# Kernel tuning notes

Hardware: AMD Instinct MI355X
Metric: run time of the kernel (lower is better)

## Reference

```python
import jax, jax.numpy as jnp
import numpy as np

B, L, T = 32, 512, 400
EMB, PRE, ENC, ARNN, DRNN, NSYM = 512, 256, 512, 1024, 1024, 256
MEAN_COEFF, SCALE_COEFF = 1.0, 10.0


def setup_inputs() -> dict:
    key = jax.random.key(0)
    ks = jax.random.split(key, 20)
    s = 0.02
    inp = {
        'memory': jax.random.normal(ks[0], (B, L, ENC), jnp.float32),
        'decoder_inputs': jax.random.normal(ks[1], (B, EMB, T), jnp.float32),
        'memory_lengths': jax.random.randint(ks[2], (B,), L // 2, L + 1).astype(jnp.int64),
        # prenet
        'pW1': jax.random.normal(ks[3], (PRE, EMB), jnp.float32) * s,
        'pb1': jnp.zeros((PRE,), jnp.float32),
        'pW2': jax.random.normal(ks[4], (PRE, PRE), jnp.float32) * s,
        'pb2': jnp.zeros((PRE,), jnp.float32),
        # attention LSTMCell
        'aWih': jax.random.normal(ks[5], (4 * ARNN, PRE + ENC), jnp.float32) * s,
        'aWhh': jax.random.normal(ks[6], (4 * ARNN, ARNN), jnp.float32) * s,
        'abih': jnp.zeros((4 * ARNN,), jnp.float32),
        'abhh': jnp.zeros((4 * ARNN,), jnp.float32),
        # Gaussian attention param linear (weight zero-init in torch; small here)
        'attWp': jax.random.normal(ks[7], (2, ARNN), jnp.float32) * 0.001,
        'attbp': jnp.zeros((2,), jnp.float32),
        # decoder LSTMCell
        'dWih': jax.random.normal(ks[8], (4 * DRNN, ARNN + ENC), jnp.float32) * s,
        'dWhh': jax.random.normal(ks[9], (4 * DRNN, DRNN), jnp.float32) * s,
        'dbih': jnp.zeros((4 * DRNN,), jnp.float32),
        'dbhh': jnp.zeros((4 * DRNN,), jnp.float32),
        # output linear
        'oW': jax.random.normal(ks[10], (NSYM, DRNN + ENC), jnp.float32) * s,
        'ob': jnp.zeros((NSYM,), jnp.float32),
    }
    return inp


def _lstm_cell(x, h, c, Wih, Whh, bih, bhh):
    g = x @ Wih.T + bih + h @ Whh.T + bhh
    i, f, gg, o = jnp.split(g, 4, axis=-1)
    c = jax.nn.sigmoid(f) * c + jax.nn.sigmoid(i) * jnp.tanh(gg)
    h = jax.nn.sigmoid(o) * jnp.tanh(c)
    return h, c


def _decoder_core(memory, decoder_inputs, memory_lengths,
                  pW1, pb1, pW2, pb2,
                  aWih, aWhh, abih, abhh,
                  attWp, attbp,
                  dWih, dWhh, dbih, dbhh,
                  oW, ob):
    b = memory.shape[0]
    Lm = memory.shape[1]
    # go frame + time-major inputs -> prenet (dropout is identity in eval)
    x = jnp.transpose(decoder_inputs, (2, 0, 1))            # [T, B, EMB]
    x = jnp.concatenate([jnp.zeros((1, b, EMB), x.dtype), x], axis=0)  # [T+1, B, EMB]
    x = jax.nn.relu(x @ pW1.T + pb1)
    x = jax.nn.relu(x @ pW2.T + pb2)                        # [T+1, B, PRE]
    x = x[:T]                                               # loop runs T steps

    lin = jnp.arange(Lm, dtype=memory.dtype)[None, :]       # [1, L]
    pad_mask = lin >= memory_lengths[:, None].astype(memory.dtype)  # [B, L] True at pad

    def step(carry, x_t):
        ah, ac, dh, dc, ctx, mean = carry
        cell_in = jnp.concatenate([x_t, ctx], axis=1)
        ah, ac = _lstm_cell(cell_in, ah, ac, aWih, aWhh, abih, abhh)
        params = ah @ attWp.T + attbp                       # [B, 2]
        mean = mean + jnp.exp(params[:, 0:1]) * MEAN_COEFF  # [B, 1]
        scale = jnp.exp(params[:, 1:2]) * SCALE_COEFF       # [B, 1]
        Z = jnp.sqrt(2.0 * np.pi * scale ** 2)
        w = jnp.exp(-0.5 * (lin - mean) ** 2 / scale ** 2) / Z  # [B, L]
        w = jnp.where(pad_mask, 0.0, w)
        ctx = jnp.einsum('bl,bld->bd', w, memory)           # [B, ENC]
        dec_in = jnp.concatenate([ah, ctx], axis=1)
        dh, dc = _lstm_cell(dec_in, dh, dc, dWih, dWhh, dbih, dbhh)
        out = jnp.concatenate([dh, ctx], axis=1) @ oW.T + ob  # [B, NSYM]
        return (ah, ac, dh, dc, ctx, mean), (out, w, params)

    z = jnp.zeros
    carry0 = (z((b, ARNN)), z((b, ARNN)), z((b, DRNN)), z((b, DRNN)),
              z((b, ENC)), z((b, 1)))
    _, (logits, aligns, ps) = jax.lax.scan(step, carry0, x)
    # time-major -> [B, T, ...]
    return (jnp.transpose(logits, (1, 0, 2)),
            jnp.transpose(aligns, (1, 0, 2)),
            jnp.transpose(ps, (1, 0, 2)))


def reference(memory, decoder_inputs, memory_lengths,
              pW1, pb1, pW2, pb2,
              aWih, aWhh, abih, abhh,
              attWp, attbp,
              dWih, dWhh, dbih, dbhh,
              oW, ob):
    return _decoder_core(memory, decoder_inputs, memory_lengths,
                         pW1, pb1, pW2, pb2,
                         aWih, aWhh, abih, abhh,
                         attWp, attbp,
                         dWih, dWhh, dbih, dbhh,
                         oW, ob)
```

## Files before the change

kernel.cpp:

```cpp
#include <hip/hip_runtime.h>
#include <math.h>

#define Bsz   32
#define Lmem  512
#define Tsteps 400
#define EMBD  512
#define PRE   256
#define ENCD  512
#define ARNN  1024
#define DRNN  1024
#define NSYM  256

typedef _Float16 f16x8 __attribute__((ext_vector_type(8)));
typedef float    f32x4 __attribute__((ext_vector_type(4)));
typedef _Float16 half_t;

#define KA2  (PRE + ENCD + ARNN)
#define KA2Q (KA2 / 4)
#define NMA2 (KA2Q / 32)
#define KD2  (ARNN + ENCD + DRNN)
#define KD2Q (KD2 / 4)
#define NMD2 (KD2Q / 32)
#define LDA_A2 1800
#define LDA_D2 2568

#define KA1  1280
#define KA1Q 320
#define NMA1 10
#define KD1  2048
#define KD1Q 512
#define NMD1 16
#define LDA_A1 1288
#define LDA_D1 2056
#define WCAP 216

__device__ __forceinline__ void st_agent_f16(half_t* p, half_t v) {
    __hip_atomic_store((unsigned short*)p, __builtin_bit_cast(unsigned short, v),
                       __ATOMIC_RELAXED, __HIP_MEMORY_SCOPE_AGENT);
}
__device__ __forceinline__ void st_agent_f32(float* p, float v) {
    __hip_atomic_store(p, v, __ATOMIC_RELAXED, __HIP_MEMORY_SCOPE_AGENT);
}
__device__ __forceinline__ void st_agent_u32(unsigned* p, unsigned v) {
    __hip_atomic_store(p, v, __ATOMIC_RELAXED, __HIP_MEMORY_SCOPE_AGENT);
}
__device__ __forceinline__ void st_agent_u64(unsigned long long* p, unsigned long long v) {
    __hip_atomic_store(p, v, __ATOMIC_RELAXED, __HIP_MEMORY_SCOPE_AGENT);
}
__device__ __forceinline__ float ld_agent_f32(const float* p) {
    return __hip_atomic_load(p, __ATOMIC_RELAXED, __HIP_MEMORY_SCOPE_AGENT);
}
__device__ __forceinline__ unsigned ld_agent_u32(const unsigned* p) {
    return __hip_atomic_load(p, __ATOMIC_RELAXED, __HIP_MEMORY_SCOPE_AGENT);
}
__device__ __forceinline__ unsigned long long ld_agent_u64(const unsigned long long* p) {
    return __hip_atomic_load(p, __ATOMIC_RELAXED, __HIP_MEMORY_SCOPE_AGENT);
}
__device__ __forceinline__ f16x8 ld_agent_f16x8(const half_t* p) {
    union { unsigned long long u[2]; f16x8 v; } c;
    c.u[0] = __hip_atomic_load((const unsigned long long*)p,
                               __ATOMIC_RELAXED, __HIP_MEMORY_SCOPE_AGENT);
    c.u[1] = __hip_atomic_load(((const unsigned long long*)p) + 1,
                               __ATOMIC_RELAXED, __HIP_MEMORY_SCOPE_AGENT);
    return c.v;
}
__device__ __forceinline__ void keep16(f16x8& v) { asm volatile("" : "+v"(v)); }

template<int KIH, int KHH>
__global__ __launch_bounds__(256) void conv_lstm_cat(
    const float* __restrict__ Wih, const float* __restrict__ Whh,
    const float* __restrict__ bih, const float* __restrict__ bhh,
    half_t* __restrict__ Wcat, float* __restrict__ bsum)
{
    constexpr int K = KIH + KHH;
    const int j = blockIdx.x;
    const float* srcA = Wih + (size_t)j * KIH;
    const float* srcB = Whh + (size_t)j * KHH;
    half_t* dst = Wcat + (size_t)j * K;
    for (int k = threadIdx.x; k < KIH; k += 256) dst[k]       = (half_t)srcA[k];
    for (int k = threadIdx.x; k < KHH; k += 256) dst[KIH + k] = (half_t)srcB[k];
    if (threadIdx.x == 0) bsum[j] = bih[j] + bhh[j];
}
template<int KIH, int KHH, int L0>
__global__ __launch_bounds__(256) void conv_lstm_skip(
    const float* __restrict__ Wih, const float* __restrict__ Whh,
    const float* __restrict__ bih, const float* __restrict__ bhh,
    half_t* __restrict__ Wcat, float* __restrict__ bsum)
{
    constexpr int K = L0 + KHH;
    const int j = blockIdx.x;
    const float* srcA = Wih + (size_t)j * KIH;
    const float* srcB = Whh + (size_t)j * KHH;
    half_t* dst = Wcat + (size_t)j * K;
    for (int k = threadIdx.x; k < L0; k += 256)  dst[k] = (half_t)srcA[k];
    for (int k = threadIdx.x; k < KHH; k += 256) dst[L0 + k] = (half_t)srcB[k];
    if (threadIdx.x == 0) bsum[j] = bih[j] + bhh[j];
}
__global__ __launch_bounds__(256) void conv_slice(
    const float* __restrict__ src, half_t* __restrict__ dst,
    int srcstride, int off, int cols)
{
    const int r = blockIdx.x;
    for (int k = threadIdx.x; k < cols; k += 256)
        dst[(size_t)r * cols + k] = (half_t)src[(size_t)r * srcstride + off + k];
}
__global__ __launch_bounds__(256) void conv_mat(
    const float* __restrict__ src, half_t* __restrict__ dst, int n)
{
    for (int i = blockIdx.x * 256 + threadIdx.x; i < n; i += gridDim.x * 256)
        dst[i] = (half_t)src[i];
}

__global__ __launch_bounds__(256) void pproj_kernel(
    const float* __restrict__ Wsrc, int Wstride, int Woff,
    const float* __restrict__ mem, half_t* __restrict__ P)
{
    const int bidx = blockIdx.x;
    const int jt  = bidx >> 9;
    const int rem = bidx & 511;
    const int lt  = rem >> 5;
    const int b   = rem & 31;
    const int tid = threadIdx.x;
    const int wave = tid >> 6, lane = tid & 63;
    const int wj = wave >> 1, wl = wave & 1;
    const int m15 = lane & 15, kh = lane >> 4;
    const int j0 = jt * 32 + wj * 16;
    const int l0 = lt * 32 + wl * 16;

    const float* wrow = Wsrc + (size_t)(j0 + m15) * Wstride + Woff + (kh << 3);
    const float* mrow = mem + ((size_t)b * Lmem + (l0 + m15)) * ENCD + (kh << 3);
    f32x4 acc = {0.f, 0.f, 0.f, 0.f};
    for (int k = 0; k < 512; k += 32) {
        float4 w0 = *(const float4*)(wrow + k);
        float4 w1 = *(const float4*)(wrow + k + 4);
        f16x8 av;
        av[0] = (half_t)w0.x; av[1] = (half_t)w0.y; av[2] = (half_t)w0.z; av[3] = (half_t)w0.w;
        av[4] = (half_t)w1.x; av[5] = (half_t)w1.y; av[6] = (half_t)w1.z; av[7] = (half_t)w1.w;
        float4 m0 = *(const float4*)(mrow + k);
        float4 m1 = *(const float4*)(mrow + k + 4);
        f16x8 bv;
        bv[0] = (half_t)m0.x; bv[1] = (half_t)m0.y; bv[2] = (half_t)m0.z; bv[3] = (half_t)m0.w;
        bv[4] = (half_t)m1.x; bv[5] = (half_t)m1.y; bv[6] = (half_t)m1.z; bv[7] = (half_t)m1.w;
        acc = __builtin_amdgcn_mfma_f32_16x16x32_f16(av, bv, acc, 0, 0, 0);
    }
    const int col = lane & 15;
    #pragma unroll
    for (int r = 0; r < 4; ++r) {
        const int row = (kh << 2) + r;
        P[((size_t)(j0 + row) * 32 + b) * 512 + (l0 + col)] = (half_t)acc[r];
    }
}

__global__ __launch_bounds__(256) void prenet_kernel(
    const float* __restrict__ din,
    const float* __restrict__ pW1, const float* __restrict__ pb1,
    const float* __restrict__ pW2, const float* __restrict__ pb2,
    half_t* __restrict__ xpre)
{
    __shared__ float xs[8][EMBD];
    __shared__ float h1s[8][PRE];
    const int tid = threadIdx.x;
    const int row0 = blockIdx.x * 8;

    for (int idx = tid; idx < 8 * EMBD; idx += 256) {
        int r = idx >> 9;
        int e = idx & 511;
        int rid = row0 + r;
        int t = rid >> 5;
        int b = rid & 31;
        float v = 0.f;
        if (t > 0) v = din[(size_t)b * EMBD * Tsteps + (size_t)e * Tsteps + (t - 1)];
        xs[r][e] = v;
    }
    __syncthreads();
    {
        float acc[8] = {0.f,0.f,0.f,0.f,0.f,0.f,0.f,0.f};
        const float* wr = pW1 + (size_t)tid * EMBD;
        for (int e = 0; e < EMBD; e += 4) {
            float4 wv = *(const float4*)(wr + e);
            #pragma unroll
            for (int r = 0; r < 8; ++r) {
                float4 xv = *(const float4*)&xs[r][e];
                acc[r] += wv.x * xv.x + wv.y * xv.y + wv.z * xv.z + wv.w * xv.w;
            }
        }
        float bias = pb1[tid];
        #pragma unroll
        for (int r = 0; r < 8; ++r) h1s[r][tid] = fmaxf(acc[r] + bias, 0.f);
    }
    __syncthreads();
    {
        float acc[8] = {0.f,0.f,0.f,0.f,0.f,0.f,0.f,0.f};
        const float* wr = pW2 + (size_t)tid * PRE;
        for (int e = 0; e < PRE; e += 4) {
            float4 wv = *(const float4*)(wr + e);
            #pragma unroll
            for (int r = 0; r < 8; ++r) {
                float4 xv = *(const float4*)&h1s[r][e];
                acc[r] += wv.x * xv.x + wv.y * xv.y + wv.z * xv.z + wv.w * xv.w;
            }
        }
        float bias = pb2[tid];
        #pragma unroll
        for (int r = 0; r < 8; ++r) {
            int rid = row0 + r;
            int t = rid >> 5;
            int b = rid & 31;
            xpre[(size_t)t * Bsz * PRE + (size_t)b * PRE + tid] =
                (half_t)fmaxf(acc[r] + bias, 0.f);
        }
    }
}

__device__ __forceinline__ void g_arrive(unsigned* flags, unsigned ph)
{
    asm volatile("s_waitcnt vmcnt(0)" ::: "memory");
    __syncthreads();
    if (threadIdx.x == 0)
        st_agent_u32(flags + blockIdx.x * 16, ph);
}
__device__ __forceinline__ void g_wait(unsigned* flags, unsigned ph)
{
    if (threadIdx.x < 64) {
        const unsigned* f = flags + threadIdx.x * 64;
        for (;;) {
            unsigned a = ld_agent_u32(f);
            unsigned b = ld_agent_u32(f + 16);
            unsigned c = ld_agent_u32(f + 32);
            unsigned d = ld_agent_u32(f + 48);
            if (min(min(a, b), min(c, d)) >= ph) break;
            __builtin_amdgcn_s_sleep(2);
        }
    }
    __syncthreads();
}

__global__ __launch_bounds__(512, 1) void decoder_2bar(
    const half_t* __restrict__ Wcat_a, const float* __restrict__ bsum_a,
    const half_t* __restrict__ Wcat_d, const float* __restrict__ bsum_d,
    const half_t* __restrict__ Wo, const float* __restrict__ ob,
    const half_t* __restrict__ xpre,
    const float* __restrict__ attWp, const float* __restrict__ attbp,
    const int* __restrict__ mlen, const half_t* __restrict__ mem16,
    half_t* __restrict__ ah0, half_t* __restrict__ ah1,
    half_t* __restrict__ dh0, half_t* __restrict__ dh1,
    half_t* __restrict__ ctx0, half_t* __restrict__ ctx1,
    float* __restrict__ mean0, float* __restrict__ mean1,
    float* __restrict__ logits, float* __restrict__ aligns,
    float* __restrict__ ps,
    unsigned* flags)
{
    const int blk   = blockIdx.x;
    const int tid   = threadIdx.x;
    const int wave  = tid >> 6;
    const int lane  = tid & 63;
    const int btile = wave & 1;
    const int kq    = wave >> 1;
    const int m15   = lane & 15;
    const int kh    = lane >> 4;
    const int u0    = blk << 2;
    const int bb    = (btile << 4) + m15;

    __shared__ __align__(16) half_t wAl[16 * LDA_A2];
    __shared__ __align__(16) half_t wDl[16 * LDA_D2];
    __shared__ float gredA[4][2][16][16];
    __shared__ float gredD[4][2][16][16];
    __shared__ float wsh[Lmem];
    __shared__ float lred[16][33];
    __shared__ float wred8[8][2];
    __shared__ float bc2[2];

    for (int g = tid; g < 16 * (KA2 / 8); g += 512) {
        int r = g / (KA2 / 8);
        int c = (g - r * (KA2 / 8)) * 8;
        int jr = (r >> 2) * 1024 + u0 + (r & 3);
        *(f16x8*)(wAl + r * LDA_A2 + c) = *(const f16x8*)(Wcat_a + (size_t)jr * KA2 + c);
    }
    for (int g = tid; g < 16 * (KD2 / 8); g += 512) {
        int r = g / (KD2 / 8);
        int c = (g - r * (KD2 / 8)) * 8;
        int jr = (r >> 2) * 1024 + u0 + (r & 3);
        *(f16x8*)(wDl + r * LDA_D2 + c) = *(const f16x8*)(Wcat_d + (size_t)jr * KD2 + c);
    }
    float bsA[4] = {0.f,0.f,0.f,0.f}, bsD[4] = {0.f,0.f,0.f,0.f};
    float cA = 0.f, cD = 0.f;
    if (tid < 128) {
        const int ul = tid >> 5;
        #pragma unroll
        for (int gi = 0; gi < 4; ++gi) bsA[gi] = bsum_a[gi * 1024 + u0 + ul];
    } else if (tid < 256) {
        const int ul = (tid - 128) >> 5;
        #pragma unroll
        for (int gi = 0; gi < 4; ++gi) bsD[gi] = bsum_d[gi * 1024 + u0 + ul];
    }
    const half_t* lA = wAl + m15 * LDA_A2 + kq * KA2Q + (kh << 3);
    const half_t* lD = wDl + m15 * LDA_D2 + kq * KD2Q + (kh << 3);
    __syncthreads();

    f16x8 bvA[NMA2], bvD[NMD2];
    {
        const half_t* s0 = xpre;
        #pragma unroll
        for (int i = 0; i < NMA2; ++i) {
            const int kg = kq * KA2Q + i * 32 + (kh << 3);
            if (kg < PRE)             bvA[i] = *(const f16x8*)(s0 + bb * PRE + kg);
            else if (kg < PRE + ENCD) bvA[i] = ld_agent_f16x8(ctx1 + bb * ENCD + (kg - PRE));
            else                      bvA[i] = ld_agent_f16x8(ah1 + bb * ARNN + (kg - PRE - ENCD));
        }
    }

    unsigned ph = 0;

    for (int t = 0; t <= Tsteps; ++t) {
        const int par = t & 1;
        half_t*       ah_cur  = par ? ah1 : ah0;
        half_t*       ctx_cur = par ? ctx1 : ctx0;
        const half_t* ctx_prv = par ? ctx0 : ctx1;
        float*        mn_cur  = par ? mean1 : mean0;
        const float*  mn_prv  = par ? mean0 : mean1;
        half_t*       dh_s    = par ? dh0 : dh1;

        if (t < Tsteps) {
            f32x4 accA = {0.f,0.f,0.f,0.f};
            #pragma unroll
            for (int i = 0; i < NMA2; ++i) {
                f16x8 av = *(const f16x8*)(lA + i * 32);
                accA = __builtin_amdgcn_mfma_f32_16x16x32_f16(av, bvA[i], accA, 0, 0, 0);
            }
            #pragma unroll
            for (int r = 0; r < 4; ++r)
                gredA[kq][btile][(kh << 2) + r][m15] = accA[r];
        }
        if (t > 0) {
            f32x4 accD = {0.f,0.f,0.f,0.f};
            #pragma unroll
            for (int i = 0; i < NMD2; ++i) {
                f16x8 av = *(const f16x8*)(lD + i * 32);
                accD = __builtin_amdgcn_mfma_f32_16x16x32_f16(av, bvD[i], accD, 0, 0, 0);
            }
            #pragma unroll
            for (int r = 0; r < 4; ++r)
                gredD[kq][btile][(kh << 2) + r][m15] = accD[r];
        }
        __syncthreads();
        if (tid < 128) {
            if (t < Tsteps) {
                const int ul = tid >> 5;
                const int bq = tid & 31;
                const int bt = bq >> 4;
                const int nn = bq & 15;
                float g[4];
                #pragma unroll
                for (int gi = 0; gi < 4; ++gi) {
                    const int mr = (gi << 2) + ul;
                    g[gi] = gredA[0][bt][mr][nn] + gredA[1][bt][mr][nn]
                          + gredA[2][bt][mr][nn] + gredA[3][bt][mr][nn] + bsA[gi];
                }
                float si = 1.f / (1.f + expf(-g[0]));
                float sf = 1.f / (1.f + expf(-g[1]));
                float so = 1.f / (1.f + expf(-g[3]));
                cA = sf * cA + si * tanhf(g[2]);
                st_agent_f16(&ah_cur[bq * 1024 + u0 + ul], (half_t)(so * tanhf(cA)));
            }
        } else if (tid < 256) {
            if (t > 0) {
                const int lt = tid - 128;
                const int ul = lt >> 5;
                const int bq = lt & 31;
                const int bt = bq >> 4;
                const int nn = bq & 15;
                float g[4];
                #pragma unroll
                for (int gi = 0; gi < 4; ++gi) {
                    const int mr = (gi << 2) + ul;
                    g[gi] = gredD[0][bt][mr][nn] + gredD[1][bt][mr][nn]
                          + gredD[2][bt][mr][nn] + gredD[3][bt][mr][nn] + bsD[gi];
                }
                float si = 1.f / (1.f + expf(-g[0]));
                float sf = 1.f / (1.f + expf(-g[1]));
                float so = 1.f / (1.f + expf(-g[3]));
                cD = sf * cD + si * tanhf(g[2]);
                st_agent_f16(&dh_s[bq * 1024 + u0 + ul], (half_t)(so * tanhf(cD)));
            }
        }
        ++ph; g_arrive(flags, ph); g_wait(flags, ph);

        if (t < Tsteps) {
            const int abt = blk >> 3;
            const int dt  = blk & 7;
            float p0, p1;
            {
                union { unsigned u; _Float16 h[2]; } a;
                a.u = ld_agent_u32((const unsigned*)(ah_cur + abt * ARNN + 2 * tid));
                float a0 = (float)a.h[0], a1 = (float)a.h[1];
                float2 w0 = *(const float2*)(attWp + 2 * tid);
                float2 w1 = *(const float2*)(attWp + ARNN + 2 * tid);
                p0 = a0 * w0.x + a1 * w0.y;
                p1 = a0 * w1.x + a1 * w1.y;
            }
            #pragma unroll
            for (int off = 32; off > 0; off >>= 1) {
                p0 += __shfl_down(p0, off, 64);
                p1 += __shfl_down(p1, off, 64);
            }
            if (lane == 0) { wred8[wave][0] = p0; wred8[wave][1] = p1; }
            __syncthreads();
            if (tid == 0) {
                float q0 = attbp[0], q1 = attbp[1];
                #pragma unroll
                for (int w = 0; w < 8; ++w) { q0 += wred8[w][0]; q1 += wred8[w][1]; }
                float mn = ld_agent_f32(&mn_prv[abt]) + expf(q0) * 1.0f;
                float sc = expf(q1) * 10.0f;
                if (dt == 0) {
                    st_agent_f32(&mn_cur[abt], mn);
                    st_agent_f32(&ps[(size_t)abt * Tsteps * 2 + (size_t)t * 2 + 0], q0);
                    st_agent_f32(&ps[(size_t)abt * Tsteps * 2 + (size_t)t * 2 + 1], q1);
                }
                bc2[0] = mn; bc2[1] = sc;
            }
            __syncthreads();
            const float mn = bc2[0], sc = bc2[1];
            const float inv_s = 1.f / sc;
            const float coef = 0.3989422804014327f * inv_s;
            const int len = mlen[abt];
            {
                float z = ((float)tid - mn) * inv_s;
                float wv = (tid < len) ? expf(-0.5f * z * z) * coef : 0.f;
                wsh[tid] = wv;
                if (dt == 0)
                    st_agent_f32(&aligns[(size_t)abt * Tsteps * Lmem + (size_t)t * Lmem + tid], wv);
            }
            __syncthreads();
            int lo = (int)fmaxf(0.f, floorf(mn - 9.f * sc));
            int hi = (int)fminf((float)len, ceilf(mn + 9.f * sc) + 1.f);
            const int d8 = (dt << 6) + (wave << 3);
            const half_t* mb = mem16 + (size_t)abt * Lmem * ENCD + d8;
            float acc[8] = {0.f,0.f,0.f,0.f,0.f,0.f,0.f,0.f};
            for (int l = lo + lane; l < hi; l += 64) {
                f16x8 mv = *(const f16x8*)(mb + (size_t)l * ENCD);
                float w = wsh[l];
                #pragma unroll
                for (int j = 0; j < 8; ++j) acc[j] += w * (float)mv[j];
            }
            #pragma unroll
            for (int off = 32; off > 0; off >>= 1) {
                #pragma unroll
                for (int j = 0; j < 8; ++j) acc[j] += __shfl_down(acc[j], off, 64);
            }
            if (lane == 0) {
                #pragma unroll
                for (int j = 0; j < 4; ++j) {
                    union { unsigned u; _Float16 h[2]; } pk;
                    pk.h[0] = (_Float16)acc[2 * j];
                    pk.h[1] = (_Float16)acc[2 * j + 1];
                    __hip_atomic_store((unsigned*)(ctx_cur + abt * ENCD + d8 + 2 * j), pk.u,
                                       __ATOMIC_RELAXED, __HIP_MEMORY_SCOPE_AGENT);
                }
            }
        }
        if (t > 0) {
            const int b_o = tid & 31;
            const int ks  = tid >> 5;
            const half_t* wrow = Wo + (size_t)blk * (DRNN + ENCD) + ks * 96;
            float outacc = 0.f;
            #pragma unroll
            for (int half = 0; half < 2; ++half) {
                f16x8 wv[6], av[6];
                #pragma unroll
                for (int c8 = 0; c8 < 6; ++c8) {
                    const int cc = half * 6 + c8;
                    const int k = ks * 96 + cc * 8;
                    wv[c8] = *(const f16x8*)(wrow + cc * 8);
                    const half_t* ap = (k < DRNN) ? (dh_s + b_o * DRNN + k)
                                                  : (ctx_prv + b_o * ENCD + (k - DRNN));
                    av[c8] = ld_agent_f16x8(ap);
                }
                #pragma unroll
                for (int c8 = 0; c8 < 6; ++c8)
                    #pragma unroll
                    for (int e = 0; e < 8; ++e)
                        outacc += (float)wv[c8][e] * (float)av[c8][e];
            }
            lred[ks][b_o] = outacc;
            __syncthreads();
            if (tid < 32) {
                float s = 0.f;
                #pragma unroll
                for (int q = 0; q < 16; ++q) s += lred[q][tid];
                st_agent_f32(&logits[(size_t)tid * Tsteps * NSYM + (size_t)(t - 1) * NSYM + blk],
                             s + ob[blk]);
            }
        }
        if (t < Tsteps) {
            ++ph; g_arrive(flags, ph);
            if (t + 1 < Tsteps) {
                const half_t* s0n = xpre + (size_t)(t + 1) * Bsz * PRE;
                #pragma unroll
                for (int i = 0; i < NMA2; ++i) {
                    const int kg = kq * KA2Q + i * 32 + (kh << 3);
                    if (kg < PRE)
                        bvA[i] = *(const f16x8*)(s0n + bb * PRE + kg);
                    else if (kg >= PRE + ENCD)
                        bvA[i] = ld_agent_f16x8(ah_cur + bb * ARNN + (kg - PRE - ENCD));
                }
            }
            #pragma unroll
            for (int i = 0; i < NMD2; ++i) {
                const int kg = kq * KD2Q + i * 32 + (kh << 3);
                if (kg < ARNN)
                    bvD[i] = ld_agent_f16x8(ah_cur + bb * ARNN + kg);
                else if (kg >= ARNN + ENCD)
                    bvD[i] = ld_agent_f16x8(dh_s + bb * DRNN + (kg - ARNN - ENCD));
            }
            #pragma unroll
            for (int i = 0; i < NMA2; ++i) keep16(bvA[i]);
            #pragma unroll
            for (int i = 0; i < NMD2; ++i) keep16(bvD[i]);
            g_wait(flags, ph);
            if (t + 1 < Tsteps) {
                #pragma unroll
                for (int i = 0; i < NMA2; ++i) {
                    const int kg = kq * KA2Q + i * 32 + (kh << 3);
                    if (kg >= PRE && kg < PRE + ENCD)
                        bvA[i] = ld_agent_f16x8(ctx_cur + bb * ENCD + (kg - PRE));
                }
            }
            #pragma unroll
            for (int i = 0; i < NMD2; ++i) {
                const int kg = kq * KD2Q + i * 32 + (kh << 3);
                if (kg >= ARNN && kg < ARNN + ENCD)
                    bvD[i] = ld_agent_f16x8(ctx_cur + bb * ENCD + (kg - ARNN));
            }
        }
    }
}

__global__ __launch_bounds__(512, 2) void decoder_1bar(
    const half_t* __restrict__ Wcat_a, const float* __restrict__ bsum_a,
    const half_t* __restrict__ Wcat_d, const float* __restrict__ bsum_d,
    const half_t* __restrict__ Wo, const float* __restrict__ ob,
    const half_t* __restrict__ xpre,
    const float* __restrict__ attWp, const float* __restrict__ attbp,
    const int* __restrict__ mlen,
    const half_t* __restrict__ P_a, const half_t* __restrict__ P_d,
    const half_t* __restrict__ P_o,
    half_t* __restrict__ ah,
    half_t* __restrict__ dh0, half_t* __restrict__ dh1,
    float* __restrict__ partials,
    float* __restrict__ logits, float* __restrict__ aligns,
    float* __restrict__ ps,
    unsigned* flags)
{
    const int blk   = blockIdx.x;
    const int tid   = threadIdx.x;
    const int wave  = tid >> 6;
    const int lane  = tid & 63;
    const int btile = wave & 1;
    const int kq    = wave >> 1;
    const int m15   = lane & 15;
    const int kh    = lane >> 4;
    const int u0    = blk << 2;
    const int bb    = (btile << 4) + m15;

    __shared__ __align__(16) half_t wAl[16 * LDA_A1];
    __shared__ __align__(16) half_t wDl[16 * LDA_D1];
    __shared__ float gredA[4][2][16][16];
    __shared__ float gredD[4][2][16][16];
    __shared__ float wshc[32][WCAP + 8];
    __shared__ float ctxA[16][32];
    __shared__ float ctxD[16][32];
    __shared__ float ctxO[32];
    __shared__ float lred[16][33];
    __shared__ float part[4][32][2];
    __shared__ float praw[32][2];
    __shared__ float bcc[32][4];
    __shared__ float bcp[32][4];
    __shared__ int   lacur[32], hicur[32];
    __shared__ int   lapv[32], hipv[32];
    __shared__ float mean32[32];
    __shared__ half_t hstA[4][32], hstD[4][32];

    for (int g = tid; g < 16 * (KA1 / 8); g += 512) {
        int r = g / (KA1 / 8);
        int c = (g - r * (KA1 / 8)) * 8;
        int jr = (r >> 2) * 1024 + u0 + (r & 3);
        *(f16x8*)(wAl + r * LDA_A1 + c) = *(const f16x8*)(Wcat_a + (size_t)jr * KA1 + c);
    }
    for (int g = tid; g < 16 * (KD1 / 8); g += 512) {
        int r = g / (KD1 / 8);
        int c = (g - r * (KD1 / 8)) * 8;
        int jr = (r >> 2) * 1024 + u0 + (r & 3);
        *(f16x8*)(wDl + r * LDA_D1 + c) = *(const f16x8*)(Wcat_d + (size_t)jr * KD1 + c);
    }
    float bsA[4] = {0.f,0.f,0.f,0.f}, bsD[4] = {0.f,0.f,0.f,0.f};
    float wp0 = 0.f, wp1 = 0.f;
    float cA = 0.f, cD = 0.f;
    if (tid < 128) {
        const int ul = tid >> 5;
        #pragma unroll
        for (int gi = 0; gi < 4; ++gi) bsA[gi] = bsum_a[gi * 1024 + u0 + ul];
        wp0 = attWp[u0 + ul];
        wp1 = attWp[ARNN + u0 + ul];
    } else if (tid < 256) {
        const int ul = (tid - 128) >> 5;
        #pragma unroll
        for (int gi = 0; gi < 4; ++gi) bsD[gi] = bsum_d[gi * 1024 + u0 + ul];
    }
    if (tid < 32) mean32[tid] = 0.f;
    const half_t* lA = wAl + m15 * LDA_A1 + kq * KA1Q + (kh << 3);
    const half_t* lD = wDl + m15 * LDA_D1 + kq * KD1Q + (kh << 3);
    __syncthreads();

    f16x8 bvA[NMA1], bvD[NMD1];
    #pragma unroll
    for (int i = 0; i < NMA1; ++i) {
        const int kg = kq * KA1Q + i * 32 + (kh << 3);
        if (kg < PRE) bvA[i] = *(const f16x8*)(xpre + bb * PRE + kg);
        else          bvA[i] = ld_agent_f16x8(ah + bb * ARNN + (kg - PRE));
    }

    unsigned ph = 0;

    for (int tau = 0; tau <= Tsteps + 1; ++tau) {
        const int par = tau & 1;
        half_t*       dhW = par ? dh1 : dh0;
        const half_t* dhR = par ? dh0 : dh1;

        if (tau >= 1) {
            if (tid < 32) {
                bcp[tid][0] = bcc[tid][0]; bcp[tid][1] = bcc[tid][1]; bcp[tid][2] = bcc[tid][2];
                lapv[tid] = lacur[tid]; hipv[tid] = hicur[tid];
            }
            __syncthreads();
        }
        if (tau >= 1 && tau <= Tsteps) {
            {
                const int b = tid >> 4, c = tid & 15;
                const unsigned long long* pb =
                    (const unsigned long long*)(partials + ((size_t)b * 256 + c * 16) * 2);
                float s0 = 0.f, s1 = 0.f;
                #pragma unroll
                for (int q = 0; q < 16; ++q) {
                    union { unsigned long long u; float2 f; } v;
                    v.u = ld_agent_u64(pb + q);
                    s0 += v.f.x; s1 += v.f.y;
                }
                s0 += __shfl_down(s0, 8, 16); s1 += __shfl_down(s1, 8, 16);
                s0 += __shfl_down(s0, 4, 16); s1 += __shfl_down(s1, 4, 16);
                s0 += __shfl_down(s0, 2, 16); s1 += __shfl_down(s1, 2, 16);
                s0 += __shfl_down(s0, 1, 16); s1 += __shfl_down(s1, 1, 16);
                if (c == 0) { praw[b][0] = s0; praw[b][1] = s1; }
            }
            __syncthreads();
            if (tid < 32) {
                float q0 = praw[tid][0] + attbp[0];
                float q1 = praw[tid][1] + attbp[1];
                float mn = mean32[tid] + expf(q0);
                mean32[tid] = mn;
                float sc = 10.f * expf(q1);
                float inv_s = 1.f / sc;
                bcc[tid][0] = mn; bcc[tid][1] = inv_s;
                bcc[tid][2] = 0.3989422804014327f * inv_s;
                int len = mlen[tid];
                int lo = (int)fmaxf(0.f, floorf(mn - 6.f * sc));
                int hi = (int)fminf((float)len, ceilf(mn + 6.f * sc) + 1.f);
                if (hi - lo > WCAP) {
                    int mid = (lo + hi) >> 1;
                    lo = mid - WCAP / 2; hi = lo + WCAP;
                    if (lo < 0) { lo = 0; hi = WCAP; }
                    if (hi > len) { hi = len; lo = hi - WCAP; if (lo < 0) lo = 0; }
                }
                if (hi < lo) hi = lo;
                lacur[tid] = lo & ~7;
                hicur[tid] = hi;
                if (blk == tid) {
                    st_agent_f32(&ps[((size_t)tid * Tsteps + (tau - 1)) * 2 + 0], q0);
                    st_agent_f32(&ps[((size_t)tid * Tsteps + (tau - 1)) * 2 + 1], q1);
                }
            }
            __syncthreads();
            {
                const int b = tid >> 4, c = tid & 15;
                const int la = lacur[b], hi = hicur[b];
                const float mn = bcc[b][0], inv_s = bcc[b][1], coef = bcc[b][2];
                for (int i = c; i < WCAP + 8; i += 16) {
                    int l = la + i;
                    float w = 0.f;
                    if (l < hi) {
                        float z = ((float)l - mn) * inv_s;
                        w = coef * expf(-0.5f * z * z);
                    }
                    wshc[b][i] = w;
                }
            }
            if (blk < 32) {
                const int len = mlen[blk];
                const float mn = bcc[blk][0], inv_s = bcc[blk][1], coef = bcc[blk][2];
                float z = ((float)tid - mn) * inv_s;
                float w = (tid < len) ? coef * expf(-0.5f * z * z) : 0.f;
                st_agent_f32(&aligns[((size_t)blk * Tsteps + (tau - 1)) * Lmem + tid], w);
            }
            __syncthreads();
        }

        if (tau < Tsteps) {
            f32x4 accA = {0.f,0.f,0.f,0.f};
            #pragma unroll
            for (int i = 0; i < NMA1; ++i) {
                f16x8 av = *(const f16x8*)(lA + i * 32);
                accA = __builtin_amdgcn_mfma_f32_16x16x32_f16(av, bvA[i], accA, 0, 0, 0);
            }
            #pragma unroll
            for (int r = 0; r < 4; ++r)
                gredA[kq][btile][(kh << 2) + r][m15] = accA[r];
        }
        if (tau >= 1 && tau <= Tsteps) {
            f32x4 accD = {0.f,0.f,0.f,0.f};
            #pragma unroll
            for (int i = 0; i < NMD1; ++i) {
                f16x8 av = *(const f16x8*)(lD + i * 32);
                accD = __builtin_amdgcn_mfma_f32_16x16x32_f16(av, bvD[i], accD, 0, 0, 0);
            }
            #pragma unroll
            for (int r = 0; r < 4; ++r)
                gredD[kq][btile][(kh << 2) + r][m15] = accD[r];
        }
        if (tau >= 2) {
            const int b_o = tid & 31;
            const int ks  = tid >> 5;
            const half_t* wrow = Wo + (size_t)blk * DRNN + ks * 64;
            const half_t* ap   = dhR + (size_t)b_o * DRNN + ks * 64;
            float outacc = 0.f;
            #pragma unroll
            for (int c8 = 0; c8 < 8; ++c8) {
                f16x8 wv = *(const f16x8*)(wrow + c8 * 8);
                f16x8 av = ld_agent_f16x8(ap + c8 * 8);
                #pragma unroll
                for (int e = 0; e < 8; ++e)
                    outacc += (float)wv[e] * (float)av[e];
            }
            lred[ks][b_o] = outacc;
        }
        if (tau >= 1 && tau <= Tsteps) {
            const int jl = tid >> 5, b = tid & 31;
            const int jg = (jl >> 2) * 1024 + u0 + (jl & 3);
            const int la = lacur[b], hi = hicur[b];
            const int nv = (hi - la + 7) >> 3;
            const half_t* pa = P_a + ((size_t)jg * 32 + b) * 512 + la;
            const half_t* pd = P_d + ((size_t)jg * 32 + b) * 512 + la;
            float sA = 0.f, sD = 0.f;
            for (int v = 0; v < nv; ++v) {
                f16x8 pav = *(const f16x8*)(pa + v * 8);
                f16x8 pdv = *(const f16x8*)(pd + v * 8);
                #pragma unroll
                for (int e = 0; e < 8; ++e) {
                    float w = wshc[b][v * 8 + e];
                    sA += w * (float)pav[e];
                    sD += w * (float)pdv[e];
                }
            }
            ctxA[jl][b] = sA;
            ctxD[jl][b] = sD;
        }
        if (tau >= 2 && tid >= 448 && tid < 480) {
            const int b = tid - 448;
            const int la = lapv[b], hi = hipv[b];
            const float mn = bcp[b][0], inv_s = bcp[b][1], coef = bcp[b][2];
            const half_t* po = P_o + ((size_t)blk * 32 + b) * 512 + la;
            float s = 0.f;
            const int nv = (hi - la + 7) >> 3;
            for (int v = 0; v < nv; ++v) {
                f16x8 pov = *(const f16x8*)(po + v * 8);
                #pragma unroll
                for (int e = 0; e < 8; ++e) {
                    int l = la + v * 8 + e;
                    if (l < hi) {
                        float z = ((float)l - mn) * inv_s;
                        s += coef * expf(-0.5f * z * z) * (float)pov[e];
                    }
                }
            }
            ctxO[b] = s;
        }
        __syncthreads();

        if (tid < 128) {
            if (tau < Tsteps) {
                const int ul = tid >> 5;
                const int bq = tid & 31;
                const int bt = bq >> 4;
                const int nn = bq & 15;
                float g[4];
                #pragma unroll
                for (int gi = 0; gi < 4; ++gi) {
                    const int mr = (gi << 2) + ul;
                    g[gi] = gredA[0][bt][mr][nn] + gredA[1][bt][mr][nn]
                          + gredA[2][bt][mr][nn] + gredA[3][bt][mr][nn] + bsA[gi]
                          + ((tau >= 1) ? ctxA[mr][bq] : 0.f);
                }
                float si = 1.f / (1.f + expf(-g[0]));
                float sf = 1.f / (1.f + expf(-g[1]));
                float so = 1.f / (1.f + expf(-g[3]));
                cA = sf * cA + si * tanhf(g[2]);
                float hval = so * tanhf(cA);
                hstA[ul][bq] = (half_t)hval;
                part[ul][bq][0] = hval * wp0;
                part[ul][bq][1] = hval * wp1;
            }
        } else if (tid < 256) {
            if (tau >= 1 && tau <= Tsteps) {
                const int lt = tid - 128;
                const int ul = lt >> 5;
                const int bq = lt & 31;
                const int bt = bq >> 4;
                const int nn = bq & 15;
                float g[4];
                #pragma unroll
                for (int gi = 0; gi < 4; ++gi) {
                    const int mr = (gi << 2) + ul;
                    g[gi] = gredD[0][bt][mr][nn] + gredD[1][bt][mr][nn]
                          + gredD[2][bt][mr][nn] + gredD[3][bt][mr][nn] + bsD[gi]
                          + ctxD[mr][bq];
                }
                float si = 1.f / (1.f + expf(-g[0]));
                float sf = 1.f / (1.f + expf(-g[1]));
                float so = 1.f / (1.f + expf(-g[3]));
                cD = sf * cD + si * tanhf(g[2]);
                hstD[ul][bq] = (half_t)(so * tanhf(cD));
            }
        } else if (tid < 288) {
            if (tau >= 2) {
                const int b = tid - 256;
                float s = 0.f;
                #pragma unroll
                for (int q = 0; q < 16; ++q) s += lred[q][b];
                st_agent_f32(&logits[(size_t)b * Tsteps * NSYM + (size_t)(tau - 2) * NSYM + blk],
                             s + ctxO[b] + ob[blk]);
            }
        }
        __syncthreads();
        if (tau < Tsteps && tid < 32) {
            union { unsigned long long u; half_t h[4]; } pk;
            #pragma unroll
            for (int q = 0; q < 4; ++q) pk.h[q] = hstA[q][tid];
            st_agent_u64((unsigned long long*)(ah + (size_t)tid * ARNN + u0), pk.u);
            float p0 = part[0][tid][0] + part[1][tid][0] + part[2][tid][0] + part[3][tid][0];
            float p1 = part[0][tid][1] + part[1][tid][1] + part[2][tid][1] + part[3][tid][1];
            union { float2 f; unsigned long long u; } pp;
            pp.f.x = p0; pp.f.y = p1;
            st_agent_u64((unsigned long long*)(partials + ((size_t)tid * 256 + blk) * 2), pp.u);
        }
        if (tau >= 1 && tau <= Tsteps && tid >= 64 && tid < 96) {
            const int b = tid - 64;
            union { unsigned long long u; half_t h[4]; } pk;
            #pragma unroll
            for (int q = 0; q < 4; ++q) pk.h[q] = hstD[q][b];
            st_agent_u64((unsigned long long*)(dhW + (size_t)b * DRNN + u0), pk.u);
        }

        if (tau <= Tsteps) {
            ++ph; g_arrive(flags, ph);
            if (tau + 1 < Tsteps) {
                const half_t* s0n = xpre + (size_t)(tau + 1) * Bsz * PRE;
                #pragma unroll
                for (int i = 0; i < NMA1; ++i) {
                    const int kg = kq * KA1Q + i * 32 + (kh << 3);
                    if (kg < PRE) { bvA[i] = *(const f16x8*)(s0n + bb * PRE + kg); keep16(bvA[i]); }
                }
            }
            g_wait(flags, ph);
            if (tau + 1 < Tsteps) {
                #pragma unroll
                for (int i = 0; i < NMA1; ++i) {
                    const int kg = kq * KA1Q + i * 32 + (kh << 3);
                    if (kg >= PRE) { bvA[i] = ld_agent_f16x8(ah + bb * ARNN + (kg - PRE)); keep16(bvA[i]); }
                }
            }
            if (tau < Tsteps) {
                #pragma unroll
                for (int i = 0; i < NMD1; ++i) {
                    const int kg = kq * KD1Q + i * 32 + (kh << 3);
                    bvD[i] = (kg < ARNN) ? ld_agent_f16x8(ah + bb * ARNN + kg)
                                         : ld_agent_f16x8(dhW + bb * DRNN + (kg - ARNN));
                    keep16(bvD[i]);
                }
            }
        }
    }
}

extern "C" void kernel_launch(void* const* d_in, const int* in_sizes, int n_in,
                              void* d_out, int out_size, void* d_ws, size_t ws_size,
                              hipStream_t stream)
{
    (void)in_sizes; (void)n_in; (void)out_size;
    const float* memory = (const float*)d_in[0];
    const float* din    = (const float*)d_in[1];
    const int*   mlen   = (const int*)d_in[2];
    const float* pW1    = (const float*)d_in[3];
    const float* pb1    = (const float*)d_in[4];
    const float* pW2    = (const float*)d_in[5];
    const float* pb2    = (const float*)d_in[6];
    const float* aWih   = (const float*)d_in[7];
    const float* aWhh   = (const float*)d_in[8];
    const float* abih   = (const float*)d_in[9];
    const float* abhh   = (const float*)d_in[10];
    const float* attWp  = (const float*)d_in[11];
    const float* attbp  = (const float*)d_in[12];
    const float* dWih   = (const float*)d_in[13];
    const float* dWhh   = (const float*)d_in[14];
    const float* dbih   = (const float*)d_in[15];
    const float* dbhh   = (const float*)d_in[16];
    const float* oW     = (const float*)d_in[17];
    const float* ob     = (const float*)d_in[18];

    float* logits = (float*)d_out;
    float* aligns = logits + (size_t)Bsz * Tsteps * NSYM;
    float* ps     = aligns + (size_t)Bsz * Tsteps * Lmem;

    char* base = (char*)d_ws;
    auto alloc = [&](size_t bytes) -> char* {
        char* p = base; base += (bytes + 255) & ~(size_t)255; return p;
    };

    if (ws_size >= ((size_t)320 << 20)) {
        half_t* Wcat_a = (half_t*)alloc((size_t)4096 * KA1 * 2);
        half_t* Wcat_d = (half_t*)alloc((size_t)4096 * KD1 * 2);
        half_t* Wo     = (half_t*)alloc((size_t)NSYM * DRNN * 2);
        float*  bsum_a = (float*)alloc(4096 * 4);
        float*  bsum_d = (float*)alloc(4096 * 4);
        half_t* xpre   = (half_t*)alloc((size_t)Tsteps * Bsz * PRE * 2);
        half_t* P_a    = (half_t*)alloc((size_t)4096 * 32 * 512 * 2);
        half_t* P_d    = (half_t*)alloc((size_t)4096 * 32 * 512 * 2);
        half_t* P_o    = (half_t*)alloc((size_t)256 * 32 * 512 * 2);
        half_t* ah     = (half_t*)alloc(Bsz * ARNN * 2);
        half_t* dh0    = (half_t*)alloc(Bsz * DRNN * 2);
        half_t* dh1    = (half_t*)alloc(Bsz * DRNN * 2);
        float*  partials = (float*)alloc((size_t)Bsz * 256 * 2 * 4);
        unsigned* flags  = (unsigned*)alloc(256 * 16 * 4);

        (void)hipMemsetAsync(ah,   0, Bsz * ARNN * 2, stream);
        (void)hipMemsetAsync(dh0,  0, Bsz * DRNN * 2, stream);
        (void)hipMemsetAsync(dh1,  0, Bsz * DRNN * 2, stream);
        (void)hipMemsetAsync(flags, 0, 256 * 16 * 4, stream);

        conv_lstm_skip<768, 1024, 256><<<4096, 256, 0, stream>>>(
            aWih, aWhh, abih, abhh, Wcat_a, bsum_a);
        conv_lstm_skip<1536, 1024, 1024><<<4096, 256, 0, stream>>>(
            dWih, dWhh, dbih, dbhh, Wcat_d, bsum_d);
        conv_slice<<<256, 256, 0, stream>>>(oW, Wo, 1536, 0, 1024);
        prenet_kernel<<<Tsteps * Bsz / 8, 256, 0, stream>>>(din, pW1, pb1, pW2, pb2, xpre);
        pproj_kernel<<<(4096 / 32) * 512, 256, 0, stream>>>(aWih, 768, 256, memory, P_a);
        pproj_kernel<<<(4096 / 32) * 512, 256, 0, stream>>>(dWih, 1536, 1024, memory, P_d);
        pproj_kernel<<<(256 / 32) * 512, 256, 0, stream>>>(oW, 1536, 1024, memory, P_o);

        decoder_1bar<<<256, 512, 0, stream>>>(
            Wcat_a, bsum_a, Wcat_d, bsum_d, Wo, ob, xpre,
            attWp, attbp, mlen, P_a, P_d, P_o,
            ah, dh0, dh1, partials,
            logits, aligns, ps, flags);
    } else {
        half_t* Wcat_a = (half_t*)alloc((size_t)4096 * KA2 * 2);
        half_t* Wcat_d = (half_t*)alloc((size_t)4096 * KD2 * 2);
        half_t* Wo     = (half_t*)alloc((size_t)NSYM * (DRNN + ENCD) * 2);
        float*  bsum_a = (float*)alloc(4096 * 4);
        float*  bsum_d = (float*)alloc(4096 * 4);
        half_t* xpre   = (half_t*)alloc((size_t)Tsteps * Bsz * PRE * 2);
        half_t* mem16  = (half_t*)alloc((size_t)Bsz * Lmem * ENCD * 2);
        half_t* ah0    = (half_t*)alloc(Bsz * ARNN * 2);
        half_t* ah1    = (half_t*)alloc(Bsz * ARNN * 2);
        half_t* dh0    = (half_t*)alloc(Bsz * DRNN * 2);
        half_t* dh1    = (half_t*)alloc(Bsz * DRNN * 2);
        half_t* ctx0   = (half_t*)alloc(Bsz * ENCD * 2);
        half_t* ctx1   = (half_t*)alloc(Bsz * ENCD * 2);
        float*  mean0  = (float*)alloc(Bsz * 4);
        float*  mean1  = (float*)alloc(Bsz * 4);
        unsigned* flags = (unsigned*)alloc(256 * 16 * 4);

        (void)hipMemsetAsync(ah1,   0, Bsz * ARNN * 2, stream);
        (void)hipMemsetAsync(dh1,   0, Bsz * DRNN * 2, stream);
        (void)hipMemsetAsync(ctx1,  0, Bsz * ENCD * 2, stream);
        (void)hipMemsetAsync(mean0, 0, Bsz * 4, stream);
        (void)hipMemsetAsync(mean1, 0, Bsz * 4, stream);
        (void)hipMemsetAsync(flags, 0, 256 * 16 * 4, stream);

        conv_lstm_cat<PRE + ENCD, ARNN><<<4096, 256, 0, stream>>>(
            aWih, aWhh, abih, abhh, Wcat_a, bsum_a);
        conv_lstm_cat<ARNN + ENCD, DRNN><<<4096, 256, 0, stream>>>(
            dWih, dWhh, dbih, dbhh, Wcat_d, bsum_d);
        conv_mat<<<768, 256, 0, stream>>>(oW, Wo, NSYM * (DRNN + ENCD));
        conv_mat<<<4096, 256, 0, stream>>>(memory, mem16, Bsz * Lmem * ENCD);
        prenet_kernel<<<Tsteps * Bsz / 8, 256, 0, stream>>>(din, pW1, pb1, pW2, pb2, xpre);

        decoder_2bar<<<256, 512, 0, stream>>>(
            Wcat_a, bsum_a, Wcat_d, bsum_d, Wo, ob, xpre,
            attWp, attbp, mlen, mem16,
            ah0, ah1, dh0, dh1, ctx0, ctx1, mean0, mean1,
            logits, aligns, ps, flags);
    }
}
```

Baseline: 14.36 ms.

## Pipeline decoder stages across timesteps with triple-buffered states and explicit context

Replaces the single-barrier decoder kernel with a version that skews the attention LSTM, decoder LSTM, context computation and output projection across consecutive timesteps. Hidden states and context live in triple buffers, so one grid barrier per step covers all stages. The precomputed memory projections for the decoder LSTM and the output layer are dropped; the context vector is instead computed directly from an fp16 copy of memory and fed to the GEMVs. This cuts the preprocessing pass and workspace size, at the cost of an explicit context reduction each step and two extra pipeline drain steps.

```diff
diff --git a/kernel.cpp b/kernel.cpp
--- a/kernel.cpp
+++ b/kernel.cpp
@@ -27,12 +27,13 @@
 #define KA1  1280
 #define KA1Q 320
 #define NMA1 10
-#define KD1  2048
-#define KD1Q 512
-#define NMD1 16
 #define LDA_A1 1288
-#define LDA_D1 2056
 #define WCAP 216
+
+#define AHN  (Bsz * ARNN)
+#define DHN  (Bsz * DRNN)
+#define CTXN (Bsz * ENCD)
+#define PARTN (Bsz * 256 * 2)
 
 __device__ __forceinline__ void st_agent_f16(half_t* p, half_t v) {
     __hip_atomic_store((unsigned short*)p, __builtin_bit_cast(unsigned short, v),
@@ -95,14 +96,6 @@
     for (int k = threadIdx.x; k < L0; k += 256)  dst[k] = (half_t)srcA[k];
     for (int k = threadIdx.x; k < KHH; k += 256) dst[L0 + k] = (half_t)srcB[k];
     if (threadIdx.x == 0) bsum[j] = bih[j] + bhh[j];
-}
-__global__ __launch_bounds__(256) void conv_slice(
-    const float* __restrict__ src, half_t* __restrict__ dst,
-    int srcstride, int off, int cols)
-{
-    const int r = blockIdx.x;
-    for (int k = threadIdx.x; k < cols; k += 256)
-        dst[(size_t)r * cols + k] = (half_t)src[(size_t)r * srcstride + off + k];
 }
 __global__ __launch_bounds__(256) void conv_mat(
     const float* __restrict__ src, half_t* __restrict__ dst, int n)
@@ -233,6 +226,366 @@
         }
     }
     __syncthreads();
+}
+
+__global__ __launch_bounds__(512, 1) void decoder_1barP(
+    const half_t* __restrict__ Wcat_a, const float* __restrict__ bsum_a,
+    const half_t* __restrict__ Wcat_d, const float* __restrict__ bsum_d,
+    const half_t* __restrict__ Wo, const float* __restrict__ ob,
+    const half_t* __restrict__ xpre,
+    const float* __restrict__ attWp, const float* __restrict__ attbp,
+    const int* __restrict__ mlen, const half_t* __restrict__ mem16,
+    const half_t* __restrict__ P_a,
+    half_t* __restrict__ ah3, half_t* __restrict__ dh3, half_t* __restrict__ ctx3,
+    float* __restrict__ partials2,
+    float* __restrict__ logits, float* __restrict__ aligns,
+    float* __restrict__ ps,
+    unsigned* flags)
+{
+    const int blk   = blockIdx.x;
+    const int tid   = threadIdx.x;
+    const int wave  = tid >> 6;
+    const int lane  = tid & 63;
+    const int btile = wave & 1;
+    const int kq    = wave >> 1;
+    const int m15   = lane & 15;
+    const int kh    = lane >> 4;
+    const int u0    = blk << 2;
+    const int bb    = (btile << 4) + m15;
+
+    __shared__ __align__(16) half_t wAl[16 * LDA_A1];
+    __shared__ __align__(16) half_t wDl[16 * LDA_D2];
+    __shared__ float gred[4][2][16][16];
+    __shared__ __align__(16) half_t wshc[32][WCAP + 8];
+    __shared__ float ctxA[16][32];
+    __shared__ float lred[16][33];
+    __shared__ float part[4][32][2];
+    __shared__ float praw[32][2];
+    __shared__ float bcc[32][4];
+    __shared__ int   lacur[32], hicur[32];
+    __shared__ float mean32[32];
+    __shared__ half_t hstA[4][32], hstD[4][32];
+
+    for (int g = tid; g < 16 * (KA1 / 8); g += 512) {
+        int r = g / (KA1 / 8);
+        int c = (g - r * (KA1 / 8)) * 8;
+        int jr = (r >> 2) * 1024 + u0 + (r & 3);
+        *(f16x8*)(wAl + r * LDA_A1 + c) = *(const f16x8*)(Wcat_a + (size_t)jr * KA1 + c);
+    }
+    for (int g = tid; g < 16 * (KD2 / 8); g += 512) {
+        int r = g / (KD2 / 8);
+        int c = (g - r * (KD2 / 8)) * 8;
+        int jr = (r >> 2) * 1024 + u0 + (r & 3);
+        *(f16x8*)(wDl + r * LDA_D2 + c) = *(const f16x8*)(Wcat_d + (size_t)jr * KD2 + c);
+    }
+    float bsA[4] = {0.f,0.f,0.f,0.f}, bsD[4] = {0.f,0.f,0.f,0.f};
+    float wp0 = 0.f, wp1 = 0.f;
+    float cA = 0.f, cD = 0.f;
+    if (tid < 128) {
+        const int ul = tid >> 5;
+        #pragma unroll
+        for (int gi = 0; gi < 4; ++gi) {
+            bsA[gi] = bsum_a[gi * 1024 + u0 + ul];
+            bsD[gi] = bsum_d[gi * 1024 + u0 + ul];
+        }
+        wp0 = attWp[u0 + ul];
+        wp1 = attWp[ARNN + u0 + ul];
+    }
+    if (tid < 32) mean32[tid] = 0.f;
+    const half_t* lA = wAl + m15 * LDA_A1 + kq * KA1Q + (kh << 3);
+    const half_t* lD = wDl + m15 * LDA_D2 + kq * KD2Q + (kh << 3);
+    __syncthreads();
+
+    f16x8 bvA[NMA1], bvD[NMD2];
+    #pragma unroll
+    for (int i = 0; i < NMA1; ++i) {
+        const int kg = kq * KA1Q + i * 32 + (kh << 3);
+        if (kg < PRE) bvA[i] = *(const f16x8*)(xpre + bb * PRE + kg);
+        else          bvA[i] = ld_agent_f16x8(ah3 + 2 * AHN + bb * ARNN + (kg - PRE));
+    }
+
+    unsigned ph = 0;
+
+    for (int tau = 0; tau <= Tsteps + 2; ++tau) {
+        half_t*       ah_w  = ah3  + (size_t)((tau + 3) % 3) * AHN;
+        const half_t* ah_r1 = ah3  + (size_t)((tau + 2) % 3) * AHN;
+        half_t*       ctx_w = ctx3 + (size_t)((tau + 2) % 3) * CTXN;
+        const half_t* ctx_o = ctx3 + (size_t)((tau) % 3) * CTXN;
+        half_t*       dh_w  = dh3  + (size_t)((tau + 1) % 3) * DHN;
+        const half_t* dh_o  = dh3  + (size_t)((tau) % 3) * DHN;
+        float*        part_w = partials2 + (size_t)(tau & 1) * PARTN;
+        const float*  part_r = partials2 + (size_t)((tau + 1) & 1) * PARTN;
+
+        if (tau >= 1 && tau <= Tsteps) {
+            {
+                const int b = tid >> 4, c = tid & 15;
+                const unsigned long long* pb =
+                    (const unsigned long long*)(part_r + ((size_t)b * 256 + c * 16) * 2);
+                float s0 = 0.f, s1 = 0.f;
+                #pragma unroll
+                for (int q = 0; q < 16; ++q) {
+                    union { unsigned long long u; float2 f; } v;
+                    v.u = ld_agent_u64(pb + q);
+                    s0 += v.f.x; s1 += v.f.y;
+                }
+                s0 += __shfl_down(s0, 8, 16); s1 += __shfl_down(s1, 8, 16);
+                s0 += __shfl_down(s0, 4, 16); s1 += __shfl_down(s1, 4, 16);
+                s0 += __shfl_down(s0, 2, 16); s1 += __shfl_down(s1, 2, 16);
+                s0 += __shfl_down(s0, 1, 16); s1 += __shfl_down(s1, 1, 16);
+                if (c == 0) { praw[b][0] = s0; praw[b][1] = s1; }
+            }
+            __syncthreads();
+            if (tid < 32) {
+                float q0 = praw[tid][0] + attbp[0];
+                float q1 = praw[tid][1] + attbp[1];
+                float mn = mean32[tid] + expf(q0);
+                mean32[tid] = mn;
+                float sc = 10.f * expf(q1);
+                float inv_s = 1.f / sc;
+                bcc[tid][0] = mn; bcc[tid][1] = inv_s;
+                bcc[tid][2] = 0.3989422804014327f * inv_s;
+                int len = mlen[tid];
+                int lo = (int)fmaxf(0.f, floorf(mn - 6.f * sc));
+                int hi = (int)fminf((float)len, ceilf(mn + 6.f * sc) + 1.f);
+                if (hi - lo > WCAP) {
+                    int mid = (lo + hi) >> 1;
+                    lo = mid - WCAP / 2; hi = lo + WCAP;
+                    if (lo < 0) { lo = 0; hi = WCAP; }
+                    if (hi > len) { hi = len; lo = hi - WCAP; if (lo < 0) lo = 0; }
+                }
+                if (hi < lo) hi = lo;
+                lacur[tid] = lo & ~7;
+                hicur[tid] = hi;
+                if (blk == tid) {
+                    st_agent_f32(&ps[((size_t)tid * Tsteps + (tau - 1)) * 2 + 0], q0);
+                    st_agent_f32(&ps[((size_t)tid * Tsteps + (tau - 1)) * 2 + 1], q1);
+                }
+            }
+            __syncthreads();
+            {
+                const int b = tid >> 4, c = tid & 15;
+                const int la = lacur[b], hi = hicur[b];
+                const float mn = bcc[b][0], inv_s = bcc[b][1], coef = bcc[b][2];
+                for (int i = c; i < WCAP + 8; i += 16) {
+                    int l = la + i;
+                    float w = 0.f;
+                    if (l < hi) {
+                        float z = ((float)l - mn) * inv_s;
+                        w = coef * expf(-0.5f * z * z);
+                    }
+                    wshc[b][i] = (half_t)w;
+                }
+            }
+            if (blk < 32) {
+                const int len = mlen[blk];
+                const float mn = bcc[blk][0], inv_s = bcc[blk][1], coef = bcc[blk][2];
+                float z = ((float)tid - mn) * inv_s;
+                float w = (tid < len) ? coef * expf(-0.5f * z * z) : 0.f;
+                st_agent_f32(&aligns[((size_t)blk * Tsteps + (tau - 1)) * Lmem + tid], w);
+            }
+            __syncthreads();
+        }
+
+        if (tau >= 1 && tau < Tsteps) {
+            const int jl = tid >> 5, b = tid & 31;
+            const int jg = (jl >> 2) * 1024 + u0 + (jl & 3);
+            const int la = lacur[b], hi = hicur[b];
+            const int nv = (hi - la + 7) >> 3;
+            const half_t* pa = P_a + ((size_t)jg * 32 + b) * 512 + la;
+            float sA = 0.f;
+            for (int v = 0; v < nv; ++v) {
+                f16x8 pav = *(const f16x8*)(pa + v * 8);
+                f16x8 wv8 = *(const f16x8*)(&wshc[b][v * 8]);
+                #pragma unroll
+                for (int e = 0; e < 8; ++e) sA += (float)wv8[e] * (float)pav[e];
+            }
+            ctxA[jl][b] = sA;
+        }
+
+        if (tau < Tsteps) {
+            f32x4 accA = {0.f,0.f,0.f,0.f};
+            #pragma unroll
+            for (int i = 0; i < NMA1; ++i) {
+                f16x8 av = *(const f16x8*)(lA + i * 32);
+                accA = __builtin_amdgcn_mfma_f32_16x16x32_f16(av, bvA[i], accA, 0, 0, 0);
+            }
+            #pragma unroll
+            for (int r = 0; r < 4; ++r)
+                gred[kq][btile][(kh << 2) + r][m15] = accA[r];
+        }
+        __syncthreads();
+        if (tau < Tsteps && tid < 128) {
+            const int ul = tid >> 5;
+            const int bq = tid & 31;
+            const int bt = bq >> 4;
+            const int nn = bq & 15;
+            float g[4];
+            #pragma unroll
+            for (int gi = 0; gi < 4; ++gi) {
+                const int mr = (gi << 2) + ul;
+                g[gi] = gred[0][bt][mr][nn] + gred[1][bt][mr][nn]
+                      + gred[2][bt][mr][nn] + gred[3][bt][mr][nn] + bsA[gi]
+                      + ((tau >= 1) ? ctxA[mr][bq] : 0.f);
+            }
+            float si = 1.f / (1.f + expf(-g[0]));
+            float sf = 1.f / (1.f + expf(-g[1]));
+            float so = 1.f / (1.f + expf(-g[3]));
+            cA = sf * cA + si * tanhf(g[2]);
+            float hval = so * tanhf(cA);
+            hstA[ul][bq] = (half_t)hval;
+            part[ul][bq][0] = hval * wp0;
+            part[ul][bq][1] = hval * wp1;
+        }
+        __syncthreads();
+        if (tau < Tsteps && tid < 32) {
+            union { unsigned long long u; half_t h[4]; } pk;
+            #pragma unroll
+            for (int q = 0; q < 4; ++q) pk.h[q] = hstA[q][tid];
+            st_agent_u64((unsigned long long*)(ah_w + (size_t)tid * ARNN + u0), pk.u);
+            float p0 = part[0][tid][0] + part[1][tid][0] + part[2][tid][0] + part[3][tid][0];
+            float p1 = part[0][tid][1] + part[1][tid][1] + part[2][tid][1] + part[3][tid][1];
+            union { float2 f; unsigned long long u; } pp;
+            pp.f.x = p0; pp.f.y = p1;
+            st_agent_u64((unsigned long long*)(part_w + ((size_t)tid * 256 + blk) * 2), pp.u);
+        }
+        if (tau >= 2 && tau <= Tsteps + 1) {
+            f32x4 accD = {0.f,0.f,0.f,0.f};
+            #pragma unroll
+            for (int i = 0; i < NMD2; ++i) {
+                f16x8 av = *(const f16x8*)(lD + i * 32);
+                accD = __builtin_amdgcn_mfma_f32_16x16x32_f16(av, bvD[i], accD, 0, 0, 0);
+            }
+            #pragma unroll
+            for (int r = 0; r < 4; ++r)
+                gred[kq][btile][(kh << 2) + r][m15] = accD[r];
+        }
+        __syncthreads();
+        if (tau >= 2 && tau <= Tsteps + 1 && tid < 128) {
+            const int ul = tid >> 5;
+            const int bq = tid & 31;
+            const int bt = bq >> 4;
+            const int nn = bq & 15;
+            float g[4];
+            #pragma unroll
+            for (int gi = 0; gi < 4; ++gi) {
+                const int mr = (gi << 2) + ul;
+                g[gi] = gred[0][bt][mr][nn] + gred[1][bt][mr][nn]
+                      + gred[2][bt][mr][nn] + gred[3][bt][mr][nn] + bsD[gi];
+            }
+            float si = 1.f / (1.f + expf(-g[0]));
+            float sf = 1.f / (1.f + expf(-g[1]));
+            float so = 1.f / (1.f + expf(-g[3]));
+            cD = sf * cD + si * tanhf(g[2]);
+            hstD[ul][bq] = (half_t)(so * tanhf(cD));
+        }
+        __syncthreads();
+        if (tau >= 2 && tau <= Tsteps + 1 && tid < 32) {
+            union { unsigned long long u; half_t h[4]; } pk;
+            #pragma unroll
+            for (int q = 0; q < 4; ++q) pk.h[q] = hstD[q][tid];
+            st_agent_u64((unsigned long long*)(dh_w + (size_t)tid * DRNN + u0), pk.u);
+        }
+        if (tau >= 1 && tau <= Tsteps) {
+            const int abt = blk >> 3, dt = blk & 7;
+            const float mn = bcc[abt][0], inv_s = bcc[abt][1], coef = bcc[abt][2];
+            const int len = mlen[abt];
+            const float sc9 = 9.f / inv_s;
+            int lo = (int)fmaxf(0.f, floorf(mn - sc9));
+            int hi = (int)fminf((float)len, ceilf(mn + sc9) + 1.f);
+            const int d8 = (dt << 6) + (wave << 3);
+            const half_t* mb = mem16 + (size_t)abt * Lmem * ENCD + d8;
+            float acc[8] = {0.f,0.f,0.f,0.f,0.f,0.f,0.f,0.f};
+            for (int l = lo + lane; l < hi; l += 64) {
+                float z = ((float)l - mn) * inv_s;
+                float w = coef * expf(-0.5f * z * z);
+                f16x8 mv = *(const f16x8*)(mb + (size_t)l * ENCD);
+                #pragma unroll
+                for (int j = 0; j < 8; ++j) acc[j] += w * (float)mv[j];
+            }
+            #pragma unroll
+            for (int off = 32; off > 0; off >>= 1) {
+                #pragma unroll
+                for (int j = 0; j < 8; ++j) acc[j] += __shfl_down(acc[j], off, 64);
+            }
+            if (lane == 0) {
+                union { unsigned long long u; half_t h[4]; } pk0, pk1;
+                #pragma unroll
+                for (int j = 0; j < 4; ++j) { pk0.h[j] = (half_t)acc[j]; pk1.h[j] = (half_t)acc[4 + j]; }
+                st_agent_u64((unsigned long long*)(ctx_w + abt * ENCD + d8), pk0.u);
+                st_agent_u64((unsigned long long*)(ctx_w + abt * ENCD + d8 + 4), pk1.u);
+            }
+        }
+        if (tau >= 3) {
+            const int b_o = tid & 31;
+            const int ks  = tid >> 5;
+            const half_t* wrow = Wo + (size_t)blk * (DRNN + ENCD) + ks * 96;
+            float outacc = 0.f;
+            #pragma unroll
+            for (int hf = 0; hf < 2; ++hf) {
+                f16x8 wv[6], av[6];
+                #pragma unroll
+                for (int c8 = 0; c8 < 6; ++c8) {
+                    const int cc = hf * 6 + c8;
+                    const int k = ks * 96 + cc * 8;
+                    wv[c8] = *(const f16x8*)(wrow + cc * 8);
+                    const half_t* ap = (k < DRNN) ? (dh_o + (size_t)b_o * DRNN + k)
+                                                  : (ctx_o + (size_t)b_o * ENCD + (k - DRNN));
+                    av[c8] = ld_agent_f16x8(ap);
+                }
+                #pragma unroll
+                for (int c8 = 0; c8 < 6; ++c8)
+                    #pragma unroll
+                    for (int e = 0; e < 8; ++e)
+                        outacc += (float)wv[c8][e] * (float)av[c8][e];
+            }
+            lred[ks][b_o] = outacc;
+            __syncthreads();
+            if (tid < 32) {
+                float s = 0.f;
+                #pragma unroll
+                for (int q = 0; q < 16; ++q) s += lred[q][tid];
+                st_agent_f32(&logits[(size_t)tid * Tsteps * NSYM + (size_t)(tau - 3) * NSYM + blk],
+                             s + ob[blk]);
+            }
+        }
+
+        if (tau <= Tsteps + 1) {
+            ++ph; g_arrive(flags, ph);
+            if (tau + 1 < Tsteps) {
+                const half_t* s0n = xpre + (size_t)(tau + 1) * Bsz * PRE;
+                #pragma unroll
+                for (int i = 0; i < NMA1; ++i) {
+                    const int kg = kq * KA1Q + i * 32 + (kh << 3);
+                    if (kg < PRE) { bvA[i] = *(const f16x8*)(s0n + bb * PRE + kg); keep16(bvA[i]); }
+                }
+            }
+            if (tau >= 1 && tau <= Tsteps) {
+                #pragma unroll
+                for (int i = 0; i < NMD2; ++i) {
+                    const int kg = kq * KD2Q + i * 32 + (kh << 3);
+                    if (kg < ARNN) { bvD[i] = ld_agent_f16x8(ah_r1 + bb * ARNN + kg); keep16(bvD[i]); }
+                }
+            }
+            g_wait(flags, ph);
+            if (tau + 1 < Tsteps) {
+                #pragma unroll
+                for (int i = 0; i < NMA1; ++i) {
+                    const int kg = kq * KA1Q + i * 32 + (kh << 3);
+                    if (kg >= PRE) { bvA[i] = ld_agent_f16x8(ah_w + bb * ARNN + (kg - PRE)); keep16(bvA[i]); }
+                }
+            }
+            if (tau >= 1 && tau <= Tsteps) {
+                #pragma unroll
+                for (int i = 0; i < NMD2; ++i) {
+                    const int kg = kq * KD2Q + i * 32 + (kh << 3);
+                    if (kg >= ARNN && kg < ARNN + ENCD)
+                        bvD[i] = ld_agent_f16x8(ctx_w + bb * ENCD + (kg - ARNN));
+                    else if (kg >= ARNN + ENCD)
+                        bvD[i] = ld_agent_f16x8(dh_w + bb * DRNN + (kg - ARNN - ENCD));
+                }
+            }
+        }
+    }
 }
 
 __global__ __launch_bounds__(512, 1) void decoder_2bar(
@@ -535,360 +888,6 @@
     }
 }
 
-__global__ __launch_bounds__(512, 2) void decoder_1bar(
-    const half_t* __restrict__ Wcat_a, const float* __restrict__ bsum_a,
-    const half_t* __restrict__ Wcat_d, const float* __restrict__ bsum_d,
-    const half_t* __restrict__ Wo, const float* __restrict__ ob,
-    const half_t* __restrict__ xpre,
-    const float* __restrict__ attWp, const float* __restrict__ attbp,
-    const int* __restrict__ mlen,
-    const half_t* __restrict__ P_a, const half_t* __restrict__ P_d,
-    const half_t* __restrict__ P_o,
-    half_t* __restrict__ ah,
-    half_t* __restrict__ dh0, half_t* __restrict__ dh1,
-    float* __restrict__ partials,
-    float* __restrict__ logits, float* __restrict__ aligns,
-    float* __restrict__ ps,
-    unsigned* flags)
-{
-    const int blk   = blockIdx.x;
-    const int tid   = threadIdx.x;
-    const int wave  = tid >> 6;
-    const int lane  = tid & 63;
-    const int btile = wave & 1;
-    const int kq    = wave >> 1;
-    const int m15   = lane & 15;
-    const int kh    = lane >> 4;
-    const int u0    = blk << 2;
-    const int bb    = (btile << 4) + m15;
-
-    __shared__ __align__(16) half_t wAl[16 * LDA_A1];
-    __shared__ __align__(16) half_t wDl[16 * LDA_D1];
-    __shared__ float gredA[4][2][16][16];
-    __shared__ float gredD[4][2][16][16];
-    __shared__ float wshc[32][WCAP + 8];
-    __shared__ float ctxA[16][32];
-    __shared__ float ctxD[16][32];
-    __shared__ float ctxO[32];
-    __shared__ float lred[16][33];
-    __shared__ float part[4][32][2];
-    __shared__ float praw[32][2];
-    __shared__ float bcc[32][4];
-    __shared__ float bcp[32][4];
-    __shared__ int   lacur[32], hicur[32];
-    __shared__ int   lapv[32], hipv[32];
-    __shared__ float mean32[32];
-    __shared__ half_t hstA[4][32], hstD[4][32];
-
-    for (int g = tid; g < 16 * (KA1 / 8); g += 512) {
-        int r = g / (KA1 / 8);
-        int c = (g - r * (KA1 / 8)) * 8;
-        int jr = (r >> 2) * 1024 + u0 + (r & 3);
-        *(f16x8*)(wAl + r * LDA_A1 + c) = *(const f16x8*)(Wcat_a + (size_t)jr * KA1 + c);
-    }
-    for (int g = tid; g < 16 * (KD1 / 8); g += 512) {
-        int r = g / (KD1 / 8);
-        int c = (g - r * (KD1 / 8)) * 8;
-        int jr = (r >> 2) * 1024 + u0 + (r & 3);
-        *(f16x8*)(wDl + r * LDA_D1 + c) = *(const f16x8*)(Wcat_d + (size_t)jr * KD1 + c);
-    }
-    float bsA[4] = {0.f,0.f,0.f,0.f}, bsD[4] = {0.f,0.f,0.f,0.f};
-    float wp0 = 0.f, wp1 = 0.f;
-    float cA = 0.f, cD = 0.f;
-    if (tid < 128) {
-        const int ul = tid >> 5;
-        #pragma unroll
-        for (int gi = 0; gi < 4; ++gi) bsA[gi] = bsum_a[gi * 1024 + u0 + ul];
-        wp0 = attWp[u0 + ul];
-        wp1 = attWp[ARNN + u0 + ul];
-    } else if (tid < 256) {
-        const int ul = (tid - 128) >> 5;
-        #pragma unroll
-        for (int gi = 0; gi < 4; ++gi) bsD[gi] = bsum_d[gi * 1024 + u0 + ul];
-    }
-    if (tid < 32) mean32[tid] = 0.f;
-    const half_t* lA = wAl + m15 * LDA_A1 + kq * KA1Q + (kh << 3);
-    const half_t* lD = wDl + m15 * LDA_D1 + kq * KD1Q + (kh << 3);
-    __syncthreads();
-
-    f16x8 bvA[NMA1], bvD[NMD1];
-    #pragma unroll
-    for (int i = 0; i < NMA1; ++i) {
-        const int kg = kq * KA1Q + i * 32 + (kh << 3);
-        if (kg < PRE) bvA[i] = *(const f16x8*)(xpre + bb * PRE + kg);
-        else          bvA[i] = ld_agent_f16x8(ah + bb * ARNN + (kg - PRE));
-    }
-
-    unsigned ph = 0;
-
-    for (int tau = 0; tau <= Tsteps + 1; ++tau) {
-        const int par = tau & 1;
-        half_t*       dhW = par ? dh1 : dh0;
-        const half_t* dhR = par ? dh0 : dh1;
-
-        if (tau >= 1) {
-            if (tid < 32) {
-                bcp[tid][0] = bcc[tid][0]; bcp[tid][1] = bcc[tid][1]; bcp[tid][2] = bcc[tid][2];
-                lapv[tid] = lacur[tid]; hipv[tid] = hicur[tid];
-            }
-            __syncthreads();
-        }
-        if (tau >= 1 && tau <= Tsteps) {
-            {
-                const int b = tid >> 4, c = tid & 15;
-                const unsigned long long* pb =
-                    (const unsigned long long*)(partials + ((size_t)b * 256 + c * 16) * 2);
-                float s0 = 0.f, s1 = 0.f;
-                #pragma unroll
-                for (int q = 0; q < 16; ++q) {
-                    union { unsigned long long u; float2 f; } v;
-                    v.u = ld_agent_u64(pb + q);
-                    s0 += v.f.x; s1 += v.f.y;
-                }
-                s0 += __shfl_down(s0, 8, 16); s1 += __shfl_down(s1, 8, 16);
-                s0 += __shfl_down(s0, 4, 16); s1 += __shfl_down(s1, 4, 16);
-                s0 += __shfl_down(s0, 2, 16); s1 += __shfl_down(s1, 2, 16);
-                s0 += __shfl_down(s0, 1, 16); s1 += __shfl_down(s1, 1, 16);
-                if (c == 0) { praw[b][0] = s0; praw[b][1] = s1; }
-            }
-            __syncthreads();
-            if (tid < 32) {
-                float q0 = praw[tid][0] + attbp[0];
-                float q1 = praw[tid][1] + attbp[1];
-                float mn = mean32[tid] + expf(q0);
-                mean32[tid] = mn;
-                float sc = 10.f * expf(q1);
-                float inv_s = 1.f / sc;
-                bcc[tid][0] = mn; bcc[tid][1] = inv_s;
-                bcc[tid][2] = 0.3989422804014327f * inv_s;
-                int len = mlen[tid];
-                int lo = (int)fmaxf(0.f, floorf(mn - 6.f * sc));
-                int hi = (int)fminf((float)len, ceilf(mn + 6.f * sc) + 1.f);
-                if (hi - lo > WCAP) {
-                    int mid = (lo + hi) >> 1;
-                    lo = mid - WCAP / 2; hi = lo + WCAP;
-                    if (lo < 0) { lo = 0; hi = WCAP; }
-                    if (hi > len) { hi = len; lo = hi - WCAP; if (lo < 0) lo = 0; }
-                }
-                if (hi < lo) hi = lo;
-                lacur[tid] = lo & ~7;
-                hicur[tid] = hi;
-                if (blk == tid) {
-                    st_agent_f32(&ps[((size_t)tid * Tsteps + (tau - 1)) * 2 + 0], q0);
-                    st_agent_f32(&ps[((size_t)tid * Tsteps + (tau - 1)) * 2 + 1], q1);
-                }
-            }
-            __syncthreads();
-            {
-                const int b = tid >> 4, c = tid & 15;
-                const int la = lacur[b], hi = hicur[b];
-                const float mn = bcc[b][0], inv_s = bcc[b][1], coef = bcc[b][2];
-                for (int i = c; i < WCAP + 8; i += 16) {
-                    int l = la + i;
-                    float w = 0.f;
-                    if (l < hi) {
-                        float z = ((float)l - mn) * inv_s;
-                        w = coef * expf(-0.5f * z * z);
-                    }
-                    wshc[b][i] = w;
-                }
-            }
-            if (blk < 32) {
-                const int len = mlen[blk];
-                const float mn = bcc[blk][0], inv_s = bcc[blk][1], coef = bcc[blk][2];
-                float z = ((float)tid - mn) * inv_s;
-                float w = (tid < len) ? coef * expf(-0.5f * z * z) : 0.f;
-                st_agent_f32(&aligns[((size_t)blk * Tsteps + (tau - 1)) * Lmem + tid], w);
-            }
-            __syncthreads();
-        }
-
-        if (tau < Tsteps) {
-            f32x4 accA = {0.f,0.f,0.f,0.f};
-            #pragma unroll
-            for (int i = 0; i < NMA1; ++i) {
-                f16x8 av = *(const f16x8*)(lA + i * 32);
-                accA = __builtin_amdgcn_mfma_f32_16x16x32_f16(av, bvA[i], accA, 0, 0, 0);
-            }
-            #pragma unroll
-            for (int r = 0; r < 4; ++r)
-                gredA[kq][btile][(kh << 2) + r][m15] = accA[r];
-        }
-        if (tau >= 1 && tau <= Tsteps) {
-            f32x4 accD = {0.f,0.f,0.f,0.f};
-            #pragma unroll
-            for (int i = 0; i < NMD1; ++i) {
-                f16x8 av = *(const f16x8*)(lD + i * 32);
-                accD = __builtin_amdgcn_mfma_f32_16x16x32_f16(av, bvD[i], accD, 0, 0, 0);
-            }
-            #pragma unroll
-            for (int r = 0; r < 4; ++r)
-                gredD[kq][btile][(kh << 2) + r][m15] = accD[r];
-        }
-        if (tau >= 2) {
-            const int b_o = tid & 31;
-            const int ks  = tid >> 5;
-            const half_t* wrow = Wo + (size_t)blk * DRNN + ks * 64;
-            const half_t* ap   = dhR + (size_t)b_o * DRNN + ks * 64;
-            float outacc = 0.f;
-            #pragma unroll
-            for (int c8 = 0; c8 < 8; ++c8) {
-                f16x8 wv = *(const f16x8*)(wrow + c8 * 8);
-                f16x8 av = ld_agent_f16x8(ap + c8 * 8);
-                #pragma unroll
-                for (int e = 0; e < 8; ++e)
-                    outacc += (float)wv[e] * (float)av[e];
-            }
-            lred[ks][b_o] = outacc;
-        }
-        if (tau >= 1 && tau <= Tsteps) {
-            const int jl = tid >> 5, b = tid & 31;
-            const int jg = (jl >> 2) * 1024 + u0 + (jl & 3);
-            const int la = lacur[b], hi = hicur[b];
-            const int nv = (hi - la + 7) >> 3;
-            const half_t* pa = P_a + ((size_t)jg * 32 + b) * 512 + la;
-            const half_t* pd = P_d + ((size_t)jg * 32 + b) * 512 + la;
-            float sA = 0.f, sD = 0.f;
-            for (int v = 0; v < nv; ++v) {
-                f16x8 pav = *(const f16x8*)(pa + v * 8);
-                f16x8 pdv = *(const f16x8*)(pd + v * 8);
-                #pragma unroll
-                for (int e = 0; e < 8; ++e) {
-                    float w = wshc[b][v * 8 + e];
-                    sA += w * (float)pav[e];
-                    sD += w * (float)pdv[e];
-                }
-            }
-            ctxA[jl][b] = sA;
-            ctxD[jl][b] = sD;
-        }
-        if (tau >= 2 && tid >= 448 && tid < 480) {
-            const int b = tid - 448;
-            const int la = lapv[b], hi = hipv[b];
-            const float mn = bcp[b][0], inv_s = bcp[b][1], coef = bcp[b][2];
-            const half_t* po = P_o + ((size_t)blk * 32 + b) * 512 + la;
-            float s = 0.f;
-            const int nv = (hi - la + 7) >> 3;
-            for (int v = 0; v < nv; ++v) {
-                f16x8 pov = *(const f16x8*)(po + v * 8);
-                #pragma unroll
-                for (int e = 0; e < 8; ++e) {
-                    int l = la + v * 8 + e;
-                    if (l < hi) {
-                        float z = ((float)l - mn) * inv_s;
-                        s += coef * expf(-0.5f * z * z) * (float)pov[e];
-                    }
-                }
-            }
-            ctxO[b] = s;
-        }
-        __syncthreads();
-
-        if (tid < 128) {
-            if (tau < Tsteps) {
-                const int ul = tid >> 5;
-                const int bq = tid & 31;
-                const int bt = bq >> 4;
-                const int nn = bq & 15;
-                float g[4];
-                #pragma unroll
-                for (int gi = 0; gi < 4; ++gi) {
-                    const int mr = (gi << 2) + ul;
-                    g[gi] = gredA[0][bt][mr][nn] + gredA[1][bt][mr][nn]
-                          + gredA[2][bt][mr][nn] + gredA[3][bt][mr][nn] + bsA[gi]
-                          + ((tau >= 1) ? ctxA[mr][bq] : 0.f);
-                }
-                float si = 1.f / (1.f + expf(-g[0]));
-                float sf = 1.f / (1.f + expf(-g[1]));
-                float so = 1.f / (1.f + expf(-g[3]));
-                cA = sf * cA + si * tanhf(g[2]);
-                float hval = so * tanhf(cA);
-                hstA[ul][bq] = (half_t)hval;
-                part[ul][bq][0] = hval * wp0;
-                part[ul][bq][1] = hval * wp1;
-            }
-        } else if (tid < 256) {
-            if (tau >= 1 && tau <= Tsteps) {
-                const int lt = tid - 128;
-                const int ul = lt >> 5;
-                const int bq = lt & 31;
-                const int bt = bq >> 4;
-                const int nn = bq & 15;
-                float g[4];
-                #pragma unroll
-                for (int gi = 0; gi < 4; ++gi) {
-                    const int mr = (gi << 2) + ul;
-                    g[gi] = gredD[0][bt][mr][nn] + gredD[1][bt][mr][nn]
-                          + gredD[2][bt][mr][nn] + gredD[3][bt][mr][nn] + bsD[gi]
-                          + ctxD[mr][bq];
-                }
-                float si = 1.f / (1.f + expf(-g[0]));
-                float sf = 1.f / (1.f + expf(-g[1]));
-                float so = 1.f / (1.f + expf(-g[3]));
-                cD = sf * cD + si * tanhf(g[2]);
-                hstD[ul][bq] = (half_t)(so * tanhf(cD));
-            }
-        } else if (tid < 288) {
-            if (tau >= 2) {
-                const int b = tid - 256;
-                float s = 0.f;
-                #pragma unroll
-                for (int q = 0; q < 16; ++q) s += lred[q][b];
-                st_agent_f32(&logits[(size_t)b * Tsteps * NSYM + (size_t)(tau - 2) * NSYM + blk],
-                             s + ctxO[b] + ob[blk]);
-            }
-        }
-        __syncthreads();
-        if (tau < Tsteps && tid < 32) {
-            union { unsigned long long u; half_t h[4]; } pk;
-            #pragma unroll
-            for (int q = 0; q < 4; ++q) pk.h[q] = hstA[q][tid];
-            st_agent_u64((unsigned long long*)(ah + (size_t)tid * ARNN + u0), pk.u);
-            float p0 = part[0][tid][0] + part[1][tid][0] + part[2][tid][0] + part[3][tid][0];
-            float p1 = part[0][tid][1] + part[1][tid][1] + part[2][tid][1] + part[3][tid][1];
-            union { float2 f; unsigned long long u; } pp;
-            pp.f.x = p0; pp.f.y = p1;
-            st_agent_u64((unsigned long long*)(partials + ((size_t)tid * 256 + blk) * 2), pp.u);
-        }
-        if (tau >= 1 && tau <= Tsteps && tid >= 64 && tid < 96) {
-            const int b = tid - 64;
-            union { unsigned long long u; half_t h[4]; } pk;
-            #pragma unroll
-            for (int q = 0; q < 4; ++q) pk.h[q] = hstD[q][b];
-            st_agent_u64((unsigned long long*)(dhW + (size_t)b * DRNN + u0), pk.u);
-        }
-
-        if (tau <= Tsteps) {
-            ++ph; g_arrive(flags, ph);
-            if (tau + 1 < Tsteps) {
-                const half_t* s0n = xpre + (size_t)(tau + 1) * Bsz * PRE;
-                #pragma unroll
-                for (int i = 0; i < NMA1; ++i) {
-                    const int kg = kq * KA1Q + i * 32 + (kh << 3);
-                    if (kg < PRE) { bvA[i] = *(const f16x8*)(s0n + bb * PRE + kg); keep16(bvA[i]); }
-                }
-            }
-            g_wait(flags, ph);
-            if (tau + 1 < Tsteps) {
-                #pragma unroll
-                for (int i = 0; i < NMA1; ++i) {
-                    const int kg = kq * KA1Q + i * 32 + (kh << 3);
-                    if (kg >= PRE) { bvA[i] = ld_agent_f16x8(ah + bb * ARNN + (kg - PRE)); keep16(bvA[i]); }
-                }
-            }
-            if (tau < Tsteps) {
-                #pragma unroll
-                for (int i = 0; i < NMD1; ++i) {
-                    const int kg = kq * KD1Q + i * 32 + (kh << 3);
-                    bvD[i] = (kg < ARNN) ? ld_agent_f16x8(ah + bb * ARNN + kg)
-                                         : ld_agent_f16x8(dhW + bb * DRNN + (kg - ARNN));
-                    keep16(bvD[i]);
-                }
-            }
-        }
-    }
-}
-
 extern "C" void kernel_launch(void* const* d_in, const int* in_sizes, int n_in,
                               void* d_out, int out_size, void* d_ws, size_t ws_size,
                               hipStream_t stream)
@@ -923,41 +922,39 @@
         char* p = base; base += (bytes + 255) & ~(size_t)255; return p;
     };
 
-    if (ws_size >= ((size_t)320 << 20)) {
+    if (ws_size >= ((size_t)192 << 20)) {
         half_t* Wcat_a = (half_t*)alloc((size_t)4096 * KA1 * 2);
-        half_t* Wcat_d = (half_t*)alloc((size_t)4096 * KD1 * 2);
-        half_t* Wo     = (half_t*)alloc((size_t)NSYM * DRNN * 2);
+        half_t* Wcat_d = (half_t*)alloc((size_t)4096 * KD2 * 2);
+        half_t* Wo     = (half_t*)alloc((size_t)NSYM * (DRNN + ENCD) * 2);
         float*  bsum_a = (float*)alloc(4096 * 4);
         float*  bsum_d = (float*)alloc(4096 * 4);
         half_t* xpre   = (half_t*)alloc((size_t)Tsteps * Bsz * PRE * 2);
+        half_t* mem16  = (half_t*)alloc((size_t)Bsz * Lmem * ENCD * 2);
         half_t* P_a    = (half_t*)alloc((size_t)4096 * 32 * 512 * 2);
-        half_t* P_d    = (half_t*)alloc((size_t)4096 * 32 * 512 * 2);
-        half_t* P_o    = (half_t*)alloc((size_t)256 * 32 * 512 * 2);
-        half_t* ah     = (half_t*)alloc(Bsz * ARNN * 2);
-        half_t* dh0    = (half_t*)alloc(Bsz * DRNN * 2);
-        half_t* dh1    = (half_t*)alloc(Bsz * DRNN * 2);
-        float*  partials = (float*)alloc((size_t)Bsz * 256 * 2 * 4);
-        unsigned* flags  = (unsigned*)alloc(256 * 16 * 4);
-
-        (void)hipMemsetAsync(ah,   0, Bsz * ARNN * 2, stream);
-        (void)hipMemsetAsync(dh0,  0, Bsz * DRNN * 2, stream);
-        (void)hipMemsetAsync(dh1,  0, Bsz * DRNN * 2, stream);
+        half_t* ah3    = (half_t*)alloc((size_t)3 * AHN * 2);
+        half_t* dh3    = (half_t*)alloc((size_t)3 * DHN * 2);
+        half_t* ctx3   = (half_t*)alloc((size_t)3 * CTXN * 2);
+        float*  partials2 = (float*)alloc((size_t)2 * PARTN * 4);
+        unsigned* flags   = (unsigned*)alloc(256 * 16 * 4);
+
+        (void)hipMemsetAsync(ah3,  0, (size_t)3 * AHN * 2, stream);
+        (void)hipMemsetAsync(dh3,  0, (size_t)3 * DHN * 2, stream);
+        (void)hipMemsetAsync(ctx3, 0, (size_t)3 * CTXN * 2, stream);
         (void)hipMemsetAsync(flags, 0, 256 * 16 * 4, stream);
 
         conv_lstm_skip<768, 1024, 256><<<4096, 256, 0, stream>>>(
             aWih, aWhh, abih, abhh, Wcat_a, bsum_a);
-        conv_lstm_skip<1536, 1024, 1024><<<4096, 256, 0, stream>>>(
+        conv_lstm_cat<1536, 1024><<<4096, 256, 0, stream>>>(
             dWih, dWhh, dbih, dbhh, Wcat_d, bsum_d);
-        conv_slice<<<256, 256, 0, stream>>>(oW, Wo, 1536, 0, 1024);
+        conv_mat<<<768, 256, 0, stream>>>(oW, Wo, NSYM * (DRNN + ENCD));
+        conv_mat<<<4096, 256, 0, stream>>>(memory, mem16, Bsz * Lmem * ENCD);
         prenet_kernel<<<Tsteps * Bsz / 8, 256, 0, stream>>>(din, pW1, pb1, pW2, pb2, xpre);
         pproj_kernel<<<(4096 / 32) * 512, 256, 0, stream>>>(aWih, 768, 256, memory, P_a);
-        pproj_kernel<<<(4096 / 32) * 512, 256, 0, stream>>>(dWih, 1536, 1024, memory, P_d);
-        pproj_kernel<<<(256 / 32) * 512, 256, 0, stream>>>(oW, 1536, 1024, memory, P_o);
-
-        decoder_1bar<<<256, 512, 0, stream>>>(
+
+        decoder_1barP<<<256, 512, 0, stream>>>(
             Wcat_a, bsum_a, Wcat_d, bsum_d, Wo, ob, xpre,
-            attWp, attbp, mlen, P_a, P_d, P_o,
-            ah, dh0, dh1, partials,
+            attWp, attbp, mlen, mem16, P_a,
+            ah3, dh3, ctx3, partials2,
             logits, aligns, ps, flags);
     } else {
         half_t* Wcat_a = (half_t*)alloc((size_t)4096 * KA2 * 2);
```

After: 22.05 ms. 53.6% more time.
